# Performance work log

Measured on AMD Instinct MI355X. Metric: run time of the kernel, lower is better.

Reference implementation:

```python
import jax, jax.numpy as jnp
import numpy as np

N, E, F_IN, H, C, G, L = 65536, 1048576, 64, 64, 10, 256, 3
BN_EPS = 1e-5


def setup_inputs() -> dict:
    key = jax.random.key(0)
    ks = jax.random.split(key, 10)
    x = jax.random.normal(ks[0], (N, F_IN), jnp.float32)
    edge_index = jax.random.randint(ks[1], (2, E), 0, N, dtype=jnp.int32)
    batch = jnp.sort(jax.random.randint(ks[2], (N,), 0, G, dtype=jnp.int32))
    # GCNConv params (stacked over L layers; F_IN == H so one stack works)
    conv_w = jax.random.normal(ks[3], (L, H, H), jnp.float32) * 0.1
    conv_b = jax.random.normal(ks[4], (L, H), jnp.float32) * 0.01
    # BatchNorm1d (eval mode: running stats)
    bn_gamma = jnp.ones((L, H), jnp.float32)
    bn_beta = jnp.zeros((L, H), jnp.float32)
    bn_mean = jax.random.normal(ks[5], (L, H), jnp.float32) * 0.01
    bn_var = jnp.ones((L, H), jnp.float32) + jax.random.uniform(ks[6], (L, H)) * 0.1
    # Classifier: Linear(H,H) -> ReLU -> Linear(H,C)
    cls_w1 = jax.random.normal(ks[7], (H, H), jnp.float32) * 0.1
    cls_b1 = jnp.zeros((H,), jnp.float32)
    cls_w2 = jax.random.normal(ks[8], (H, C), jnp.float32) * 0.1
    cls_b2 = jnp.zeros((C,), jnp.float32)
    return dict(x=x, conv_w=conv_w, conv_b=conv_b, bn_gamma=bn_gamma,
                bn_beta=bn_beta, bn_mean=bn_mean, bn_var=bn_var,
                cls_w1=cls_w1, cls_b1=cls_b1, cls_w2=cls_w2, cls_b2=cls_b2,
                edge_index=edge_index, batch=batch)


def _gcn_conv(h, w, b, src, dst, dis):
    # GCNConv with self-loops and symmetric normalization D^-1/2 (A+I) D^-1/2
    h = h @ w                                   # [N, H]
    coef = dis[src] * dis[dst]                  # [E]
    agg = jnp.zeros_like(h).at[dst].add(h[src] * coef[:, None])
    agg = agg + h * (dis * dis)[:, None]        # self-loop term
    return agg + b


def reference(x, conv_w, conv_b, bn_gamma, bn_beta, bn_mean, bn_var,
              cls_w1, cls_b1, cls_w2, cls_b2, edge_index, batch):
    src, dst = edge_index[0], edge_index[1]
    # degree with self-loops (counted on target index, as in PyG)
    deg = jnp.ones((N,), x.dtype).at[dst].add(1.0)
    dis = jax.lax.rsqrt(deg)
    h = x
    for i in range(L):
        res = h if i > 0 else None
        h = _gcn_conv(h, conv_w[i], conv_b[i], src, dst, dis)
        # BatchNorm1d (eval) + ReLU  (dropout is identity in eval mode)
        h = bn_gamma[i] * (h - bn_mean[i]) * jax.lax.rsqrt(bn_var[i] + BN_EPS) + bn_beta[i]
        h = jax.nn.relu(h)
        if res is not None:  # dims always match (H == H)
            h = h + res
    # global_mean_pool
    counts = jnp.zeros((G,), x.dtype).at[batch].add(1.0)
    sums = jax.ops.segment_sum(h, batch, num_segments=G)
    graph_repr = sums / jnp.maximum(counts, 1.0)[:, None]   # [G, H]
    z = jax.nn.relu(graph_repr @ cls_w1 + cls_b1)
    logits = z @ cls_w2 + cls_b2
    return jax.nn.log_softmax(logits, axis=1)
```

## Files before the change

kernel.cpp:

```cpp
#include <hip/hip_runtime.h>
#include <hip/hip_fp16.h>
#include <math.h>

#define N_NODES 65536
#define N_EDGES 1048576
#define HDIM 64
#define NCLS 10
#define NGRAPH 256
#define NLAYER 3
#define BN_EPS 1e-5f
#define NBUCKET 256
#define NPBLK 256


__global__ __launch_bounds__(256) void hist_kernel(const int* __restrict__ dst,
                                                   unsigned* __restrict__ bhist) {
    __shared__ unsigned hist[NBUCKET];
    int b = blockIdx.x, tid = threadIdx.x;
    hist[tid] = 0;
    __syncthreads();
    int base = b * 4096;
#pragma unroll
    for (int k = 0; k < 16; ++k) {
        int d = dst[base + k * 256 + tid];
        atomicAdd(&hist[d >> 8], 1u);
    }
    __syncthreads();
    bhist[tid * NPBLK + b] = hist[tid];
}


__global__ __launch_bounds__(256) void scan1_kernel(const unsigned* __restrict__ in,
                                                    unsigned* __restrict__ out,
                                                    unsigned* __restrict__ bsum) {
    __shared__ unsigned lds[256];
    int t = threadIdx.x, b = blockIdx.x;
    unsigned v = in[b * 256 + t];
    lds[t] = v;
    __syncthreads();
#pragma unroll
    for (int off = 1; off < 256; off <<= 1) {
        unsigned add = (t >= off) ? lds[t - off] : 0u;
        __syncthreads();
        lds[t] += add;
        __syncthreads();
    }
    out[b * 256 + t] = lds[t] - v;
    if (t == 255) bsum[b] = lds[255];
}

__global__ __launch_bounds__(256) void scan2_kernel(const unsigned* __restrict__ bsum,
                                                    unsigned* __restrict__ carry) {
    __shared__ unsigned lds[256];
    int t = threadIdx.x;
    unsigned v = bsum[t];
    lds[t] = v;
    __syncthreads();
#pragma unroll
    for (int off = 1; off < 256; off <<= 1) {
        unsigned add = (t >= off) ? lds[t - off] : 0u;
        __syncthreads();
        lds[t] += add;
        __syncthreads();
    }
    carry[t] = lds[t] - v;
}

__global__ __launch_bounds__(256) void scan3_kernel(unsigned* __restrict__ out,
                                                    const unsigned* __restrict__ carry) {
    int i = blockIdx.x * 256 + threadIdx.x;
    out[i] += carry[i >> 8];
}


__global__ __launch_bounds__(256) void partition_kernel(const int* __restrict__ ei,
                                                        const unsigned* __restrict__ bpos,
                                                        int2* __restrict__ ebuf) {
    __shared__ unsigned cur[NBUCKET];
    int b = blockIdx.x, tid = threadIdx.x;
    cur[tid] = bpos[tid * NPBLK + b];
    __syncthreads();
    int base = b * 4096;
#pragma unroll
    for (int k = 0; k < 16; ++k) {
        int e = base + k * 256 + tid;
        int s = ei[e];
        int d = ei[N_EDGES + e];
        unsigned slot = atomicAdd(&cur[d >> 8], 1u);
        ebuf[slot] = make_int2(s, d);
    }
}


__global__ __launch_bounds__(256) void csr_kernel(const int2* __restrict__ ebuf,
                                                  const unsigned* __restrict__ bpos,
                                                  unsigned* __restrict__ offsets,
                                                  float* __restrict__ dis,
                                                  int* __restrict__ srcs) {
    __shared__ unsigned hist[NBUCKET];
    __shared__ unsigned scn[NBUCKET];
    int B = blockIdx.x, tid = threadIdx.x;
    unsigned start = bpos[B * NPBLK];
    unsigned end = (B == NBUCKET - 1) ? N_EDGES : bpos[(B + 1) * NPBLK];
    hist[tid] = 0;
    __syncthreads();
    for (unsigned e = start + tid; e < end; e += 256)
        atomicAdd(&hist[ebuf[e].y & 255], 1u);
    __syncthreads();
    unsigned v = hist[tid];
    scn[tid] = v;
    __syncthreads();
#pragma unroll
    for (int off = 1; off < 256; off <<= 1) {
        unsigned add = (tid >= off) ? scn[tid - off] : 0u;
        __syncthreads();
        scn[tid] += add;
        __syncthreads();
    }
    unsigned gbase = start + scn[tid] - v;
    int node = B * 256 + tid;
    offsets[node] = gbase;
    dis[node] = rsqrtf((float)(v + 1u));
    if (B == NBUCKET - 1 && tid == 255) offsets[N_NODES] = N_EDGES;
    hist[tid] = gbase;
    __syncthreads();
    for (unsigned e = start + tid; e < end; e += 256) {
        int2 ed = ebuf[e];
        unsigned slot = atomicAdd(&hist[ed.y & 255], 1u);
        srcs[slot] = ed.x;
    }
}


__global__ __launch_bounds__(256) void prep_bn_kernel(const float* __restrict__ bias,
                                                      const float* __restrict__ gamma,
                                                      const float* __restrict__ beta,
                                                      const float* __restrict__ mean,
                                                      const float* __restrict__ var,
                                                      float* __restrict__ scb,
                                                      float* __restrict__ shb) {
    int t = threadIdx.x;
    if (t < NLAYER * HDIM) {
        float sc = gamma[t] * rsqrtf(var[t] + BN_EPS);
        scb[t] = sc;
        shb[t] = (bias[t] - mean[t]) * sc + beta[t];
    }
}


__global__ __launch_bounds__(256) void gemm_kernel(const float* __restrict__ hin,
                                                   const float* __restrict__ W,
                                                   const float* __restrict__ dis,
                                                   __half* __restrict__ hw16) {
    __shared__ float hs[64][68];
    __shared__ float ws[64 * 64];
    int tid = threadIdx.x;
    int row0 = blockIdx.x * 64;

    {
        const float4* Wv = (const float4*)W;
        float4* wsv = (float4*)ws;
#pragma unroll
        for (int i = 0; i < 4; ++i) wsv[tid + i * 256] = Wv[tid + i * 256];
    }
    {
        const float4* Hv = (const float4*)(hin + (size_t)row0 * HDIM);
#pragma unroll
        for (int i = 0; i < 4; ++i) {
            int idx = tid + i * 256;
            int r = idx >> 4;
            int c = (idx & 15) << 2;
            *(float4*)&hs[r][c] = Hv[idx];
        }
    }
    __syncthreads();

    int tx = tid & 15, ty = tid >> 4;
    float acc[4][4] = {};
#pragma unroll
    for (int kq = 0; kq < 16; ++kq) {
        int k = kq * 4;
        float4 a[4], b[4];
#pragma unroll
        for (int i = 0; i < 4; ++i) a[i] = *(const float4*)&hs[ty * 4 + i][k];
#pragma unroll
        for (int kk = 0; kk < 4; ++kk) b[kk] = *(const float4*)&ws[(k + kk) * 64 + tx * 4];
#pragma unroll
        for (int kk = 0; kk < 4; ++kk) {
            float b0 = b[kk].x, b1 = b[kk].y, b2 = b[kk].z, b3 = b[kk].w;
#pragma unroll
            for (int i = 0; i < 4; ++i) {
                float av = (kk == 0) ? a[i].x : (kk == 1) ? a[i].y : (kk == 2) ? a[i].z : a[i].w;
                acc[i][0] += av * b0;
                acc[i][1] += av * b1;
                acc[i][2] += av * b2;
                acc[i][3] += av * b3;
            }
        }
    }

#pragma unroll
    for (int i = 0; i < 4; ++i) {
        int row = row0 + ty * 4 + i;
        float dd = dis[row];
        __half2 pa = __floats2half2_rn(acc[i][0] * dd, acc[i][1] * dd);
        __half2 pb = __floats2half2_rn(acc[i][2] * dd, acc[i][3] * dd);
        uint2 pk;
        pk.x = *(unsigned*)&pa;
        pk.y = *(unsigned*)&pb;
        *(uint2*)&hw16[(size_t)row * HDIM + tx * 4] = pk;
    }
}


__global__ __launch_bounds__(256) void aggregate_kernel(const __half* __restrict__ hw16,
                                                        const float* __restrict__ dis,
                                                        const unsigned* __restrict__ offsets,
                                                        const int* __restrict__ srcs,
                                                        const float* __restrict__ scb,
                                                        const float* __restrict__ shb,
                                                        float* __restrict__ h,
                                                        int has_res) {
    int n = (blockIdx.x * 256 + threadIdx.x) >> 6;
    int lane = threadIdx.x & 63;
    int eslot = lane >> 3;
    int fl = lane & 7;
    int e0 = (int)offsets[n];
    int e1 = (int)offsets[n + 1];

    const uint4* hv = (const uint4*)hw16;

    float4 accA = make_float4(0.f, 0.f, 0.f, 0.f);
    float4 accB = make_float4(0.f, 0.f, 0.f, 0.f);
    int e = e0 + eslot;
    for (; e + 8 < e1; e += 16) {
        int s0 = srcs[e];
        int s1 = srcs[e + 8];
        uint4 r0 = hv[(size_t)s0 * 8 + fl];
        uint4 r1 = hv[(size_t)s1 * 8 + fl];
        {
            float2 p0 = __half22float2(*(__half2*)&r0.x);
            float2 p1 = __half22float2(*(__half2*)&r0.y);
            float2 p2 = __half22float2(*(__half2*)&r0.z);
            float2 p3 = __half22float2(*(__half2*)&r0.w);
            accA.x += p0.x; accA.y += p0.y; accA.z += p1.x; accA.w += p1.y;
            accB.x += p2.x; accB.y += p2.y; accB.z += p3.x; accB.w += p3.y;
        }
        {
            float2 p0 = __half22float2(*(__half2*)&r1.x);
            float2 p1 = __half22float2(*(__half2*)&r1.y);
            float2 p2 = __half22float2(*(__half2*)&r1.z);
            float2 p3 = __half22float2(*(__half2*)&r1.w);
            accA.x += p0.x; accA.y += p0.y; accA.z += p1.x; accA.w += p1.y;
            accB.x += p2.x; accB.y += p2.y; accB.z += p3.x; accB.w += p3.y;
        }
    }
    if (e < e1) {
        int s0 = srcs[e];
        uint4 r0 = hv[(size_t)s0 * 8 + fl];
        float2 p0 = __half22float2(*(__half2*)&r0.x);
        float2 p1 = __half22float2(*(__half2*)&r0.y);
        float2 p2 = __half22float2(*(__half2*)&r0.z);
        float2 p3 = __half22float2(*(__half2*)&r0.w);
        accA.x += p0.x; accA.y += p0.y; accA.z += p1.x; accA.w += p1.y;
        accB.x += p2.x; accB.y += p2.y; accB.z += p3.x; accB.w += p3.y;
    }
#pragma unroll
    for (int m = 8; m <= 32; m <<= 1) {
        accA.x += __shfl_xor(accA.x, m); accA.y += __shfl_xor(accA.y, m);
        accA.z += __shfl_xor(accA.z, m); accA.w += __shfl_xor(accA.w, m);
        accB.x += __shfl_xor(accB.x, m); accB.y += __shfl_xor(accB.y, m);
        accB.z += __shfl_xor(accB.z, m); accB.w += __shfl_xor(accB.w, m);
    }
    if (lane < 8) {
        uint4 rs = hv[(size_t)n * 8 + fl];
        float2 p0 = __half22float2(*(__half2*)&rs.x);
        float2 p1 = __half22float2(*(__half2*)&rs.y);
        float2 p2 = __half22float2(*(__half2*)&rs.z);
        float2 p3 = __half22float2(*(__half2*)&rs.w);
        accA.x += p0.x; accA.y += p0.y; accA.z += p1.x; accA.w += p1.y;
        accB.x += p2.x; accB.y += p2.y; accB.z += p3.x; accB.w += p3.y;
        float d = dis[n];
        float4 scA = ((const float4*)scb)[fl * 2];
        float4 scB = ((const float4*)scb)[fl * 2 + 1];
        float4 shA = ((const float4*)shb)[fl * 2];
        float4 shB = ((const float4*)shb)[fl * 2 + 1];
        float o0 = fmaxf(accA.x * d * scA.x + shA.x, 0.0f);
        float o1 = fmaxf(accA.y * d * scA.y + shA.y, 0.0f);
        float o2 = fmaxf(accA.z * d * scA.z + shA.z, 0.0f);
        float o3 = fmaxf(accA.w * d * scA.w + shA.w, 0.0f);
        float o4 = fmaxf(accB.x * d * scB.x + shB.x, 0.0f);
        float o5 = fmaxf(accB.y * d * scB.y + shB.y, 0.0f);
        float o6 = fmaxf(accB.z * d * scB.z + shB.z, 0.0f);
        float o7 = fmaxf(accB.w * d * scB.w + shB.w, 0.0f);
        float* hp = &h[(size_t)n * HDIM + fl * 8];
        if (has_res) {
            float4 rA = *(const float4*)hp;
            float4 rB = *(const float4*)(hp + 4);
            o0 += rA.x; o1 += rA.y; o2 += rA.z; o3 += rA.w;
            o4 += rB.x; o5 += rB.y; o6 += rB.z; o7 += rB.w;
        }
        *(float4*)hp = make_float4(o0, o1, o2, o3);
        *(float4*)(hp + 4) = make_float4(o4, o5, o6, o7);
    }
}


__device__ __forceinline__ int lower_bound_batch(const int* __restrict__ batch, int val) {
    int lo = 0, hi = N_NODES;
    while (lo < hi) {
        int mid = (lo + hi) >> 1;
        if (batch[mid] < val) lo = mid + 1; else hi = mid;
    }
    return lo;
}

__global__ __launch_bounds__(256) void pool_classify_kernel(const float* __restrict__ h,
                                                            const int* __restrict__ batch,
                                                            const float* __restrict__ w1,
                                                            const float* __restrict__ b1,
                                                            const float* __restrict__ w2,
                                                            const float* __restrict__ b2,
                                                            float* __restrict__ out) {
    int g = blockIdx.x;
    int tid = threadIdx.x;
    int start = lower_bound_batch(batch, g);
    int end = lower_bound_batch(batch, g + 1);
    int f = tid & 63;
    int grp = tid >> 6;
    float s0 = 0.f, s1 = 0.f, s2 = 0.f, s3 = 0.f;
    int n = start + grp;
    for (; n + 12 < end; n += 16) {
        s0 += h[(size_t)n * HDIM + f];
        s1 += h[(size_t)(n + 4) * HDIM + f];
        s2 += h[(size_t)(n + 8) * HDIM + f];
        s3 += h[(size_t)(n + 12) * HDIM + f];
    }
    for (; n < end; n += 4) s0 += h[(size_t)n * HDIM + f];
    float s = (s0 + s1) + (s2 + s3);
    __shared__ float red[4][64];
    __shared__ float repr[64], z[64], lg[NCLS];
    red[grp][f] = s;
    __syncthreads();
    if (grp == 0) {
        float tot = red[0][f] + red[1][f] + red[2][f] + red[3][f];
        int cnt = end - start;
        repr[f] = tot / (float)(cnt > 0 ? cnt : 1);
    }
    __syncthreads();
    if (tid < 64) {
        float acc = b1[tid];
#pragma unroll 8
        for (int k = 0; k < HDIM; ++k) acc += repr[k] * w1[k * HDIM + tid];
        z[tid] = fmaxf(acc, 0.0f);
    }
    __syncthreads();
    if (tid < NCLS) {
        float a2 = b2[tid];
#pragma unroll 8
        for (int k = 0; k < HDIM; ++k) a2 += z[k] * w2[k * NCLS + tid];
        lg[tid] = a2;
    }
    __syncthreads();
    if (tid < NCLS) {
        float m = -1e30f;
#pragma unroll
        for (int c = 0; c < NCLS; ++c) m = fmaxf(m, lg[c]);
        float sum = 0.0f;
#pragma unroll
        for (int c = 0; c < NCLS; ++c) sum += expf(lg[c] - m);
        out[g * NCLS + tid] = lg[tid] - m - logf(sum);
    }
}


extern "C" void kernel_launch(void* const* d_in, const int* in_sizes, int n_in,
                              void* d_out, int out_size, void* d_ws, size_t ws_size,
                              hipStream_t stream) {
    const float* x        = (const float*)d_in[0];
    const float* conv_w   = (const float*)d_in[1];
    const float* conv_b   = (const float*)d_in[2];
    const float* bn_gamma = (const float*)d_in[3];
    const float* bn_beta  = (const float*)d_in[4];
    const float* bn_mean  = (const float*)d_in[5];
    const float* bn_var   = (const float*)d_in[6];
    const float* cls_w1   = (const float*)d_in[7];
    const float* cls_b1   = (const float*)d_in[8];
    const float* cls_w2   = (const float*)d_in[9];
    const float* cls_b2   = (const float*)d_in[10];
    const int* edge_index = (const int*)d_in[11];
    const int* batch      = (const int*)d_in[12];
    float* out = (float*)d_out;

    char* ws = (char*)d_ws;
    unsigned* bhist   = (unsigned*)(ws);
    unsigned* bpos    = (unsigned*)(ws + (256u << 10));
    unsigned* bsum    = (unsigned*)(ws + (512u << 10));
    unsigned* carry   = (unsigned*)(ws + (513u << 10));
    float*    scb     = (float*)(ws + (514u << 10));
    float*    shb     = (float*)(ws + (515u << 10));
    float*    dis     = (float*)(ws + (768u << 10));
    unsigned* offsets = (unsigned*)(ws + (1u << 20));
    int2*     ebuf    = (int2*)(ws + (2u << 20));
    int*      srcs    = (int*)(ws + (10u << 20));
    __half*   hw16    = (__half*)(ws + (14u << 20));
    float*    h       = (float*)(ws + (22u << 20));

    hist_kernel<<<NPBLK, 256, 0, stream>>>(edge_index + N_EDGES, bhist);
    scan1_kernel<<<(NBUCKET * NPBLK) / 256, 256, 0, stream>>>(bhist, bpos, bsum);
    scan2_kernel<<<1, 256, 0, stream>>>(bsum, carry);
    scan3_kernel<<<(NBUCKET * NPBLK) / 256, 256, 0, stream>>>(bpos, carry);
    partition_kernel<<<NPBLK, 256, 0, stream>>>(edge_index, bpos, ebuf);
    csr_kernel<<<NBUCKET, 256, 0, stream>>>(ebuf, bpos, offsets, dis, srcs);
    prep_bn_kernel<<<1, 256, 0, stream>>>(conv_b, bn_gamma, bn_beta, bn_mean, bn_var, scb, shb);

    for (int l = 0; l < NLAYER; ++l) {
        const float* hin = (l == 0) ? x : h;
        gemm_kernel<<<N_NODES / 64, 256, 0, stream>>>(hin, conv_w + l * HDIM * HDIM, dis, hw16);
        aggregate_kernel<<<(N_NODES * 64) / 256, 256, 0, stream>>>(
            hw16, dis, offsets, srcs, scb + l * HDIM, shb + l * HDIM, h, (l > 0) ? 1 : 0);
    }

    pool_classify_kernel<<<NGRAPH, 256, 0, stream>>>(h, batch, cls_w1, cls_b1, cls_w2, cls_b2, out);
}
```

Measured before the change: 191.4 us.

## Pack edge records into 32 bits, use 16-bit sources, split aggregation by feature half

Each partitioned edge is now packed into a single 32-bit word (dst<<16 | src), and the CSR source array is stored as 16-bit indices. This halves the edge buffer and source-index traffic. The scan3 and prep_bn kernels are removed: their work is folded into scan2, and carry is added where bpos is read. The aggregation kernel now runs two passes via blockIdx.y, each covering half the features with 16 edge slots per node, which raises parallelism per node but re-reads offsets and source indices twice.

```diff
diff --git a/kernel.cpp b/kernel.cpp
--- a/kernel.cpp
+++ b/kernel.cpp
@@ -50,7 +50,14 @@
 }
 
 __global__ __launch_bounds__(256) void scan2_kernel(const unsigned* __restrict__ bsum,
-                                                    unsigned* __restrict__ carry) {
+                                                    unsigned* __restrict__ carry,
+                                                    const float* __restrict__ bias,
+                                                    const float* __restrict__ gamma,
+                                                    const float* __restrict__ beta,
+                                                    const float* __restrict__ mean,
+                                                    const float* __restrict__ var,
+                                                    float* __restrict__ scb,
+                                                    float* __restrict__ shb) {
     __shared__ unsigned lds[256];
     int t = threadIdx.x;
     unsigned v = bsum[t];
@@ -64,21 +71,21 @@
         __syncthreads();
     }
     carry[t] = lds[t] - v;
-}
-
-__global__ __launch_bounds__(256) void scan3_kernel(unsigned* __restrict__ out,
-                                                    const unsigned* __restrict__ carry) {
-    int i = blockIdx.x * 256 + threadIdx.x;
-    out[i] += carry[i >> 8];
+    if (t < NLAYER * HDIM) {
+        float sc = gamma[t] * rsqrtf(var[t] + BN_EPS);
+        scb[t] = sc;
+        shb[t] = (bias[t] - mean[t]) * sc + beta[t];
+    }
 }
 
 
 __global__ __launch_bounds__(256) void partition_kernel(const int* __restrict__ ei,
                                                         const unsigned* __restrict__ bpos,
-                                                        int2* __restrict__ ebuf) {
+                                                        const unsigned* __restrict__ carry,
+                                                        unsigned* __restrict__ ebuf) {
     __shared__ unsigned cur[NBUCKET];
     int b = blockIdx.x, tid = threadIdx.x;
-    cur[tid] = bpos[tid * NPBLK + b];
+    cur[tid] = bpos[tid * NPBLK + b] + carry[tid];
     __syncthreads();
     int base = b * 4096;
 #pragma unroll
@@ -87,25 +94,26 @@
         int s = ei[e];
         int d = ei[N_EDGES + e];
         unsigned slot = atomicAdd(&cur[d >> 8], 1u);
-        ebuf[slot] = make_int2(s, d);
-    }
-}
-
-
-__global__ __launch_bounds__(256) void csr_kernel(const int2* __restrict__ ebuf,
+        ebuf[slot] = ((unsigned)d << 16) | (unsigned)s;
+    }
+}
+
+
+__global__ __launch_bounds__(256) void csr_kernel(const unsigned* __restrict__ ebuf,
                                                   const unsigned* __restrict__ bpos,
+                                                  const unsigned* __restrict__ carry,
                                                   unsigned* __restrict__ offsets,
                                                   float* __restrict__ dis,
-                                                  int* __restrict__ srcs) {
+                                                  unsigned short* __restrict__ srcs) {
     __shared__ unsigned hist[NBUCKET];
     __shared__ unsigned scn[NBUCKET];
     int B = blockIdx.x, tid = threadIdx.x;
-    unsigned start = bpos[B * NPBLK];
-    unsigned end = (B == NBUCKET - 1) ? N_EDGES : bpos[(B + 1) * NPBLK];
+    unsigned start = bpos[B * NPBLK] + carry[B];
+    unsigned end = (B == NBUCKET - 1) ? N_EDGES : (bpos[(B + 1) * NPBLK] + carry[B + 1]);
     hist[tid] = 0;
     __syncthreads();
     for (unsigned e = start + tid; e < end; e += 256)
-        atomicAdd(&hist[ebuf[e].y & 255], 1u);
+        atomicAdd(&hist[(ebuf[e] >> 16) & 255], 1u);
     __syncthreads();
     unsigned v = hist[tid];
     scn[tid] = v;
@@ -125,25 +133,9 @@
     hist[tid] = gbase;
     __syncthreads();
     for (unsigned e = start + tid; e < end; e += 256) {
-        int2 ed = ebuf[e];
-        unsigned slot = atomicAdd(&hist[ed.y & 255], 1u);
-        srcs[slot] = ed.x;
-    }
-}
-
-
-__global__ __launch_bounds__(256) void prep_bn_kernel(const float* __restrict__ bias,
-                                                      const float* __restrict__ gamma,
-                                                      const float* __restrict__ beta,
-                                                      const float* __restrict__ mean,
-                                                      const float* __restrict__ var,
-                                                      float* __restrict__ scb,
-                                                      float* __restrict__ shb) {
-    int t = threadIdx.x;
-    if (t < NLAYER * HDIM) {
-        float sc = gamma[t] * rsqrtf(var[t] + BN_EPS);
-        scb[t] = sc;
-        shb[t] = (bias[t] - mean[t]) * sc + beta[t];
+        unsigned ed = ebuf[e];
+        unsigned slot = atomicAdd(&hist[(ed >> 16) & 255], 1u);
+        srcs[slot] = (unsigned short)(ed & 0xFFFFu);
     }
 }
 
@@ -216,15 +208,17 @@
 __global__ __launch_bounds__(256) void aggregate_kernel(const __half* __restrict__ hw16,
                                                         const float* __restrict__ dis,
                                                         const unsigned* __restrict__ offsets,
-                                                        const int* __restrict__ srcs,
+                                                        const unsigned short* __restrict__ srcs,
                                                         const float* __restrict__ scb,
                                                         const float* __restrict__ shb,
                                                         float* __restrict__ h,
                                                         int has_res) {
     int n = (blockIdx.x * 256 + threadIdx.x) >> 6;
     int lane = threadIdx.x & 63;
-    int eslot = lane >> 3;
-    int fl = lane & 7;
+    int pass = blockIdx.y;
+    int eslot = lane >> 2;
+    int fl = lane & 3;
+    int hbase = pass * 4 + fl;
     int e0 = (int)offsets[n];
     int e1 = (int)offsets[n + 1];
 
@@ -232,32 +226,9 @@
 
     float4 accA = make_float4(0.f, 0.f, 0.f, 0.f);
     float4 accB = make_float4(0.f, 0.f, 0.f, 0.f);
-    int e = e0 + eslot;
-    for (; e + 8 < e1; e += 16) {
+    for (int e = e0 + eslot; e < e1; e += 16) {
         int s0 = srcs[e];
-        int s1 = srcs[e + 8];
-        uint4 r0 = hv[(size_t)s0 * 8 + fl];
-        uint4 r1 = hv[(size_t)s1 * 8 + fl];
-        {
-            float2 p0 = __half22float2(*(__half2*)&r0.x);
-            float2 p1 = __half22float2(*(__half2*)&r0.y);
-            float2 p2 = __half22float2(*(__half2*)&r0.z);
-            float2 p3 = __half22float2(*(__half2*)&r0.w);
-            accA.x += p0.x; accA.y += p0.y; accA.z += p1.x; accA.w += p1.y;
-            accB.x += p2.x; accB.y += p2.y; accB.z += p3.x; accB.w += p3.y;
-        }
-        {
-            float2 p0 = __half22float2(*(__half2*)&r1.x);
-            float2 p1 = __half22float2(*(__half2*)&r1.y);
-            float2 p2 = __half22float2(*(__half2*)&r1.z);
-            float2 p3 = __half22float2(*(__half2*)&r1.w);
-            accA.x += p0.x; accA.y += p0.y; accA.z += p1.x; accA.w += p1.y;
-            accB.x += p2.x; accB.y += p2.y; accB.z += p3.x; accB.w += p3.y;
-        }
-    }
-    if (e < e1) {
-        int s0 = srcs[e];
-        uint4 r0 = hv[(size_t)s0 * 8 + fl];
+        uint4 r0 = hv[(size_t)s0 * 8 + hbase];
         float2 p0 = __half22float2(*(__half2*)&r0.x);
         float2 p1 = __half22float2(*(__half2*)&r0.y);
         float2 p2 = __half22float2(*(__half2*)&r0.z);
@@ -266,14 +237,14 @@
         accB.x += p2.x; accB.y += p2.y; accB.z += p3.x; accB.w += p3.y;
     }
 #pragma unroll
-    for (int m = 8; m <= 32; m <<= 1) {
+    for (int m = 4; m <= 32; m <<= 1) {
         accA.x += __shfl_xor(accA.x, m); accA.y += __shfl_xor(accA.y, m);
         accA.z += __shfl_xor(accA.z, m); accA.w += __shfl_xor(accA.w, m);
         accB.x += __shfl_xor(accB.x, m); accB.y += __shfl_xor(accB.y, m);
         accB.z += __shfl_xor(accB.z, m); accB.w += __shfl_xor(accB.w, m);
     }
-    if (lane < 8) {
-        uint4 rs = hv[(size_t)n * 8 + fl];
+    if (lane < 4) {
+        uint4 rs = hv[(size_t)n * 8 + hbase];
         float2 p0 = __half22float2(*(__half2*)&rs.x);
         float2 p1 = __half22float2(*(__half2*)&rs.y);
         float2 p2 = __half22float2(*(__half2*)&rs.z);
@@ -281,10 +252,11 @@
         accA.x += p0.x; accA.y += p0.y; accA.z += p1.x; accA.w += p1.y;
         accB.x += p2.x; accB.y += p2.y; accB.z += p3.x; accB.w += p3.y;
         float d = dis[n];
-        float4 scA = ((const float4*)scb)[fl * 2];
-        float4 scB = ((const float4*)scb)[fl * 2 + 1];
-        float4 shA = ((const float4*)shb)[fl * 2];
-        float4 shB = ((const float4*)shb)[fl * 2 + 1];
+        int off = pass * 32 + fl * 8;
+        float4 scA = *(const float4*)&scb[off];
+        float4 scB = *(const float4*)&scb[off + 4];
+        float4 shA = *(const float4*)&shb[off];
+        float4 shB = *(const float4*)&shb[off + 4];
         float o0 = fmaxf(accA.x * d * scA.x + shA.x, 0.0f);
         float o1 = fmaxf(accA.y * d * scA.y + shA.y, 0.0f);
         float o2 = fmaxf(accA.z * d * scA.z + shA.z, 0.0f);
@@ -293,7 +265,7 @@
         float o5 = fmaxf(accB.y * d * scB.y + shB.y, 0.0f);
         float o6 = fmaxf(accB.z * d * scB.z + shB.z, 0.0f);
         float o7 = fmaxf(accB.w * d * scB.w + shB.w, 0.0f);
-        float* hp = &h[(size_t)n * HDIM + fl * 8];
+        float* hp = &h[(size_t)n * HDIM + off];
         if (has_res) {
             float4 rA = *(const float4*)hp;
             float4 rB = *(const float4*)(hp + 4);
@@ -393,31 +365,30 @@
     float* out = (float*)d_out;
 
     char* ws = (char*)d_ws;
-    unsigned* bhist   = (unsigned*)(ws);
-    unsigned* bpos    = (unsigned*)(ws + (256u << 10));
-    unsigned* bsum    = (unsigned*)(ws + (512u << 10));
-    unsigned* carry   = (unsigned*)(ws + (513u << 10));
-    float*    scb     = (float*)(ws + (514u << 10));
-    float*    shb     = (float*)(ws + (515u << 10));
-    float*    dis     = (float*)(ws + (768u << 10));
-    unsigned* offsets = (unsigned*)(ws + (1u << 20));
-    int2*     ebuf    = (int2*)(ws + (2u << 20));
-    int*      srcs    = (int*)(ws + (10u << 20));
-    __half*   hw16    = (__half*)(ws + (14u << 20));
-    float*    h       = (float*)(ws + (22u << 20));
+    unsigned*       bhist   = (unsigned*)(ws);
+    unsigned*       bpos    = (unsigned*)(ws + (256u << 10));
+    unsigned*       bsum    = (unsigned*)(ws + (512u << 10));
+    unsigned*       carry   = (unsigned*)(ws + (513u << 10));
+    float*          scb     = (float*)(ws + (514u << 10));
+    float*          shb     = (float*)(ws + (515u << 10));
+    float*          dis     = (float*)(ws + (768u << 10));
+    unsigned*       offsets = (unsigned*)(ws + (1u << 20));
+    unsigned*       ebuf    = (unsigned*)(ws + (2u << 20));
+    unsigned short* srcs    = (unsigned short*)(ws + (6u << 20));
+    __half*         hw16    = (__half*)(ws + (8u << 20));
+    float*          h       = (float*)(ws + (16u << 20));
 
     hist_kernel<<<NPBLK, 256, 0, stream>>>(edge_index + N_EDGES, bhist);
     scan1_kernel<<<(NBUCKET * NPBLK) / 256, 256, 0, stream>>>(bhist, bpos, bsum);
-    scan2_kernel<<<1, 256, 0, stream>>>(bsum, carry);
-    scan3_kernel<<<(NBUCKET * NPBLK) / 256, 256, 0, stream>>>(bpos, carry);
-    partition_kernel<<<NPBLK, 256, 0, stream>>>(edge_index, bpos, ebuf);
-    csr_kernel<<<NBUCKET, 256, 0, stream>>>(ebuf, bpos, offsets, dis, srcs);
-    prep_bn_kernel<<<1, 256, 0, stream>>>(conv_b, bn_gamma, bn_beta, bn_mean, bn_var, scb, shb);
+    scan2_kernel<<<1, 256, 0, stream>>>(bsum, carry, conv_b, bn_gamma, bn_beta,
+                                        bn_mean, bn_var, scb, shb);
+    partition_kernel<<<NPBLK, 256, 0, stream>>>(edge_index, bpos, carry, ebuf);
+    csr_kernel<<<NBUCKET, 256, 0, stream>>>(ebuf, bpos, carry, offsets, dis, srcs);
 
     for (int l = 0; l < NLAYER; ++l) {
         const float* hin = (l == 0) ? x : h;
         gemm_kernel<<<N_NODES / 64, 256, 0, stream>>>(hin, conv_w + l * HDIM * HDIM, dis, hw16);
-        aggregate_kernel<<<(N_NODES * 64) / 256, 256, 0, stream>>>(
+        aggregate_kernel<<<dim3((N_NODES * 64) / 256, 2), 256, 0, stream>>>(
             hw16, dis, offsets, srcs, scb + l * HDIM, shb + l * HDIM, h, (l > 0) ? 1 : 0);
     }
 
```

Result: slower. 255.1 us (+33.3%).
